# Performance work log

Hardware: AMD Instinct MI355X
Metric: run time of the kernel (lower is better)

The kernel has to match this reference:

```python
import jax, jax.numpy as jnp
import numpy as np

NUM_NODES = 100000
NUM_EDGES = 3_200_000
WALKS_PER_NODE = 4
WALK_LENGTH = 8
SKIP_FIRST = True


def setup_inputs() -> dict:
    key = jax.random.key(0)
    k1, k2, k3 = jax.random.split(key, 3)
    edge_index = jax.random.randint(k1, (2, NUM_EDGES), 0, NUM_NODES, dtype=jnp.int32)
    edge_weight = jax.random.uniform(k2, (NUM_EDGES,), dtype=jnp.float32)
    # one uniform per walker per step; S = NUM_NODES * WALKS_PER_NODE
    rand_unif = jax.random.uniform(k3, (NUM_NODES * WALKS_PER_NODE, WALK_LENGTH), dtype=jnp.float32)
    return {"edge_index": edge_index, "edge_weight": edge_weight, "rand_unif": rand_unif}


def _random_walk_edges(edge_index, rand_unif):
    """Returns added [2, S*L] edges (root -> walked node), int dtype."""
    row, col = edge_index[0], edge_index[1]
    # is_sorted=False path: sort edges by source to build CSR
    order = jnp.argsort(row)
    row_s = row[order]
    col_s = col[order]
    deg = jax.ops.segment_sum(jnp.ones_like(row_s), row_s, num_segments=NUM_NODES)  # [N]
    rowptr = jnp.concatenate([jnp.zeros((1,), deg.dtype), jnp.cumsum(deg)])  # [N+1]
    # start = all nodes, repeated walks_per_node times
    start = jnp.tile(jnp.arange(NUM_NODES, dtype=row.dtype), WALKS_PER_NODE)  # [S]

    def step(cur, u):
        d = deg[cur]  # [S]
        off = jnp.minimum((u * d.astype(u.dtype)).astype(cur.dtype), jnp.maximum(d - 1, 0))
        nxt = jnp.where(d > 0, col_s[rowptr[cur] + off], cur)  # stay if isolated
        return nxt, nxt

    _, walks = jax.lax.scan(step, start, rand_unif.T)  # [L_total, S]
    walks = walks.T  # [S, WALK_LENGTH] == n_id[:, 1:]
    k = 1 if SKIP_FIRST else 0  # skip_first drops the first-hop node (n_id[:, 2:])
    targets = walks[:, k:]  # [S, L]
    L = targets.shape[1]
    roots = jnp.broadcast_to(start[:, None], (start.shape[0], L))
    return jnp.stack([roots.reshape(-1), targets.reshape(-1)])  # [2, S*L]


def reference(edge_index, edge_weight, rand_unif):
    added = _random_walk_edges(edge_index, rand_unif)
    out_edge_index = jnp.concatenate([edge_index, added], axis=1)
    added_w = jnp.ones((added.shape[1],), edge_weight.dtype)
    out_edge_weight = jnp.concatenate([edge_weight, added_w])
    return out_edge_index, out_edge_weight
```

## Files before the change

kernel.cpp:

```cpp
#include <hip/hip_runtime.h>

#define ARW_N_NODES   100000
#define ARW_N_EDGES   3200000
#define ARW_N_WALKERS 400000
#define ARW_WLEN      8
#define ARW_LOUT      7
#define ARW_ROW_LEN   6000000
#define ARW_OUT_ELEMS 18000000

#define ARW_NB    256
#define ARW_RPB   392
#define ARW_NT    3125
#define ARW_TP    3136
#define ARW_TILE  1024
#define ARW_TPB   25

#define ARW_HT    0
#define ARW_BT    900000
#define ARW_TOT   1750000
#define ARW_CB    1760000
#define ARW_PD    1800000
#define ARW_P     6000000
#define ARW_COLS  12000000

__global__ void AddRandomWalkEdge_16896401342869_kernel() {}

__global__ __launch_bounds__(1024) void arw16896_thist(const int* __restrict__ row,
                                                       int* __restrict__ s) {
    __shared__ int h[ARW_TPB * 256];
    int tid = threadIdx.x;
    for (int x = tid; x < ARW_TPB * 256; x += 1024) h[x] = 0;
    __syncthreads();
    int base_e = blockIdx.x * (ARW_TPB * ARW_TILE) + tid;
    #pragma unroll
    for (int j = 0; j < ARW_TPB; j++)
        atomicAdd(&h[j * 256 + (row[base_e + j * 1024] / ARW_RPB)], 1);
    __syncthreads();
    for (int x = tid; x < ARW_TPB * ARW_NB; x += 1024) {
        int b = x / ARW_TPB, j = x % ARW_TPB;
        s[ARW_HT + b * ARW_TP + blockIdx.x * ARW_TPB + j] = h[j * 256 + b];
    }
}

__global__ __launch_bounds__(1024) void arw16896_btot(int* __restrict__ s) {
    __shared__ int wsum[16];
    int b = blockIdx.x, tid = threadIdx.x, lane = tid & 63, wid = tid >> 6;
    int acc = 0;
    for (int t = tid; t < ARW_NT; t += 1024) acc += s[ARW_HT + b * ARW_TP + t];
    #pragma unroll
    for (int off = 32; off > 0; off >>= 1) acc += __shfl_down(acc, off, 64);
    if (lane == 0) wsum[wid] = acc;
    __syncthreads();
    if (tid == 0) {
        int a = 0;
        #pragma unroll
        for (int w = 0; w < 16; w++) a += wsum[w];
        s[ARW_TOT + b] = a;
    }
}

__global__ __launch_bounds__(256) void arw16896_bbase(int* __restrict__ s) {
    __shared__ int sm[256];
    int tid = threadIdx.x;
    int v = s[ARW_TOT + tid];
    sm[tid] = v;
    __syncthreads();
    for (int off = 1; off < 256; off <<= 1) {
        int x = 0;
        if (tid >= off) x = sm[tid - off];
        __syncthreads();
        sm[tid] += x;
        __syncthreads();
    }
    s[ARW_CB + tid] = sm[tid] - v;
}

__global__ __launch_bounds__(1024) void arw16896_bscan2(int* __restrict__ s) {
    __shared__ int wsum[16];
    int b = blockIdx.x, tid = threadIdx.x, lane = tid & 63, wid = tid >> 6;
    int carry = s[ARW_CB + b];
    for (int c0 = 0; c0 < ARW_NT; c0 += 1024) {
        int t = c0 + tid;
        int v = (t < ARW_NT) ? s[ARW_HT + b * ARW_TP + t] : 0;
        int sv = v;
        #pragma unroll
        for (int off = 1; off < 64; off <<= 1) {
            int x = __shfl_up(sv, off, 64);
            if (lane >= off) sv += x;
        }
        if (lane == 63) wsum[wid] = sv;
        __syncthreads();
        int pre = 0, tot = 0;
        #pragma unroll
        for (int w = 0; w < 16; w++) {
            int x = wsum[w];
            if (w < wid) pre += x;
            tot += x;
        }
        if (t < ARW_NT) s[ARW_BT + b * ARW_TP + t] = carry + pre + sv - v;
        carry += tot;
        __syncthreads();
    }
}

__global__ __launch_bounds__(1024) void arw16896_part(const int* __restrict__ row,
                                                      const int* __restrict__ col,
                                                      int* __restrict__ s) {
    __shared__ unsigned W[16 * 256];
    int tid  = threadIdx.x;
    int wave = tid >> 6, lane = tid & 63;
    int e = blockIdx.x * ARW_TILE + tid;
    int r = row[e], cv = col[e];
    int b = r / ARW_RPB;
    int lr = r - b * ARW_RPB;
    W[tid] = 0; W[tid + 1024] = 0; W[tid + 2048] = 0; W[tid + 3072] = 0;
    __syncthreads();
    unsigned long long mask = ~0ULL;
    #pragma unroll
    for (int bit = 0; bit < 8; bit++) {
        unsigned long long bal = __ballot((b >> bit) & 1);
        mask &= ((b >> bit) & 1) ? bal : ~bal;
    }
    int rankw = __popcll(mask & ((1ULL << lane) - 1ULL));
    W[wave * 256 + b] = (unsigned)__popcll(mask);
    __syncthreads();
    int cross = 0;
    for (int w2 = 0; w2 < 16; w2++) {
        if (w2 >= wave) break;
        cross += (int)W[w2 * 256 + b];
    }
    int base = s[ARW_BT + b * ARW_TP + blockIdx.x];
    s[ARW_P + base + cross + rankw] = (lr << 17) | cv;
}

__global__ __launch_bounds__(1024) void arw16896_pass2(int* __restrict__ s) {
    __shared__ unsigned W[16 * 512];
    __shared__ int hist[512], pref[512], runc[512];
    int tid = threadIdx.x, lane = tid & 63, wave = tid >> 6;
    int b = blockIdx.x;
    int start = s[ARW_BT + b * ARW_TP];
    int end   = (b == ARW_NB - 1) ? ARW_N_EDGES : s[ARW_BT + (b + 1) * ARW_TP];
    int cnt = end - start;
    int rows0 = b * ARW_RPB;
    int nrows = ARW_N_NODES - rows0; if (nrows > ARW_RPB) nrows = ARW_RPB;

    if (tid < 512) hist[tid] = 0;
    __syncthreads();
    for (int k = tid; k < cnt; k += 1024)
        atomicAdd(&hist[(unsigned)s[ARW_P + start + k] >> 17], 1);
    __syncthreads();
    if (tid < 512) pref[tid] = hist[tid];
    __syncthreads();
    for (int off = 1; off < 512; off <<= 1) {
        int x = 0;
        if (tid < 512 && tid >= off) x = pref[tid - off];
        __syncthreads();
        if (tid < 512) pref[tid] += x;
        __syncthreads();
    }
    if (tid < 512) runc[tid] = 0;
    if (tid < nrows) {
        unsigned deg = (unsigned)hist[tid];
        unsigned rp  = (unsigned)(start + pref[tid] - hist[tid]);
        s[ARW_PD + rows0 + tid] = (int)((rp << 10) | deg);
    }
    __syncthreads();

    for (int c0 = 0; c0 < cnt; c0 += 1024) {
        int k = c0 + tid;
        int valid = (k < cnt) ? 1 : 0;
        unsigned p = valid ? (unsigned)s[ARW_P + start + k] : 0u;
        unsigned lr = p >> 17;
        #pragma unroll
        for (int j = 0; j < 8; j++) W[tid + j * 1024] = 0;
        __syncthreads();
        unsigned long long mask = ~0ULL;
        #pragma unroll
        for (int bit = 0; bit < 9; bit++) {
            unsigned long long bal = __ballot((lr >> bit) & 1u);
            mask &= ((lr >> bit) & 1u) ? bal : ~bal;
        }
        mask &= __ballot(valid);
        int rankw = __popcll(mask & ((1ULL << lane) - 1ULL));
        if (valid) W[wave * 512 + lr] = (unsigned)__popcll(mask);
        __syncthreads();
        if (valid) {
            int cross = 0;
            for (int w2 = 0; w2 < 16; w2++) {
                if (w2 >= wave) break;
                cross += (int)W[w2 * 512 + lr];
            }
            int pos = start + (pref[lr] - hist[lr]) + runc[lr] + cross + rankw;
            s[ARW_COLS + pos] = (int)(p & 0x1FFFFu);
        }
        __syncthreads();
        if (tid < 512) {
            int a = 0;
            #pragma unroll
            for (int w = 0; w < 16; w++) a += (int)W[w * 512 + tid];
            runc[tid] += a;
        }
        __syncthreads();
    }
}

__global__ __launch_bounds__(64) void arw16896_walk(const float* __restrict__ ru,
                                                    const int* __restrict__ s,
                                                    float* __restrict__ o) {
    __shared__ float tg[4 * 64 * ARW_LOUT];
    int tid = threadIdx.x;
    int v = blockIdx.x * 64 + tid;
    if (v < ARW_N_NODES) {
        float uu[4][8];
        int cur[4];
        #pragma unroll
        for (int k = 0; k < 4; k++) {
            const float4* rp4 = (const float4*)(ru + (size_t)(v + k * ARW_N_NODES) * 8);
            float4 ra = rp4[0], rb = rp4[1];
            uu[k][0] = ra.x; uu[k][1] = ra.y; uu[k][2] = ra.z; uu[k][3] = ra.w;
            uu[k][4] = rb.x; uu[k][5] = rb.y; uu[k][6] = rb.z; uu[k][7] = rb.w;
        }
        unsigned pd0 = (unsigned)s[ARW_PD + v];
        int d0  = (int)(pd0 & 1023u);
        int rp0 = (int)(pd0 >> 10);
        #pragma unroll
        for (int k = 0; k < 4; k++) {
            int off = (int)(uu[k][0] * (float)d0);
            if (off > d0 - 1) off = d0 - 1;
            int nxt = s[ARW_COLS + rp0 + off];
            cur[k] = (d0 > 0) ? nxt : v;
        }
        #pragma unroll
        for (int t = 1; t < ARW_WLEN; t++) {
            unsigned pdk[4];
            #pragma unroll
            for (int k = 0; k < 4; k++) pdk[k] = (unsigned)s[ARW_PD + cur[k]];
            #pragma unroll
            for (int k = 0; k < 4; k++) {
                int d = (int)(pdk[k] & 1023u);
                int off = (int)(uu[k][t] * (float)d);
                if (off > d - 1) off = d - 1;
                int nxt = s[ARW_COLS + (int)(pdk[k] >> 10) + off];
                cur[k] = (d > 0) ? nxt : cur[k];
                tg[k * (64 * ARW_LOUT) + tid * ARW_LOUT + (t - 1)] = (float)cur[k];
            }
        }
    }
    __syncthreads();
    int blkN = ARW_N_NODES - blockIdx.x * 64;
    if (blkN > 64) blkN = 64;
    int valid = blkN * ARW_LOUT;
    #pragma unroll
    for (int k = 0; k < 4; k++) {
        int base = ARW_ROW_LEN + ARW_N_EDGES +
                   (k * ARW_N_NODES + blockIdx.x * 64) * ARW_LOUT;
        for (int j = tid; j < valid; j += 64)
            o[base + j] = tg[k * (64 * ARW_LOUT) + j];
    }
}

__global__ __launch_bounds__(256) void arw16896_asm(const int* __restrict__ ei,
                                                    const float* __restrict__ wgt,
                                                    float* __restrict__ o) {
    int i4 = blockIdx.x * blockDim.x + threadIdx.x;
    if (i4 < ARW_N_EDGES / 4) {
        int4 r0 = ((const int4*)ei)[i4];
        int4 r1 = ((const int4*)(ei + ARW_N_EDGES))[i4];
        float4 wv = ((const float4*)wgt)[i4];
        ((float4*)o)[i4] = make_float4((float)r0.x, (float)r0.y, (float)r0.z, (float)r0.w);
        ((float4*)(o + ARW_ROW_LEN))[i4] =
            make_float4((float)r1.x, (float)r1.y, (float)r1.z, (float)r1.w);
        ((float4*)(o + 2 * ARW_ROW_LEN))[i4] = wv;
    }
    if (i4 < (ARW_N_WALKERS * ARW_LOUT) / 4) {
        int i = i4 * 4;
        float4 r;
        r.x = (float)(((i    ) / ARW_LOUT) % ARW_N_NODES);
        r.y = (float)(((i + 1) / ARW_LOUT) % ARW_N_NODES);
        r.z = (float)(((i + 2) / ARW_LOUT) % ARW_N_NODES);
        r.w = (float)(((i + 3) / ARW_LOUT) % ARW_N_NODES);
        ((float4*)(o + ARW_N_EDGES))[i4] = r;
        ((float4*)(o + 2 * ARW_ROW_LEN + ARW_N_EDGES))[i4] = make_float4(1.f, 1.f, 1.f, 1.f);
    }
}

extern "C" void kernel_launch(void* const* d_in, const int* in_sizes, int n_in,
                              void* d_out, int out_size, void* d_ws, size_t ws_size,
                              hipStream_t stream) {
    const int*   ei  = (const int*)d_in[0];
    const float* wgt = (const float*)d_in[1];
    const float* ru  = (const float*)d_in[2];
    int*   s = (int*)d_out;
    float* o = (float*)d_out;
    const int* row = ei;
    const int* col = ei + ARW_N_EDGES;

    arw16896_thist <<<ARW_NT / ARW_TPB, 1024, 0, stream>>>(row, s);
    arw16896_btot  <<<ARW_NB, 1024, 0, stream>>>(s);
    arw16896_bbase <<<1, 256, 0, stream>>>(s);
    arw16896_bscan2<<<ARW_NB, 1024, 0, stream>>>(s);
    arw16896_part  <<<ARW_NT, 1024, 0, stream>>>(row, col, s);
    arw16896_pass2 <<<ARW_NB, 1024, 0, stream>>>(s);
    arw16896_walk  <<<(ARW_N_NODES + 63) / 64, 64, 0, stream>>>(ru, s, o);
    arw16896_asm   <<<(ARW_N_EDGES / 4 + 255) / 256, 256, 0, stream>>>(ei, wgt, o);
}
```

Baseline: 252.8 us.

## Merge bucket scan passes, stage pass2 in LDS, fuse assembly into walk

The separate bucket-total kernel is folded into the per-bucket scan, which now produces local offsets plus a total. The partition kernel adds the global bucket base itself, which removes one kernel launch. The thist tiles-per-block count drops to 5 to get more blocks. pass2 stages its bucket's packed entries in shared memory so they are read from global memory once, and the W counters shrink to 16-bit. The walk kernel moves to 256-thread blocks and also writes the col-row conversion and the root indices, which trims the work of the assembly kernel. The larger shared memory footprint in pass2 and walk may lower occupancy.

```diff
diff --git a/kernel.cpp b/kernel.cpp
--- a/kernel.cpp
+++ b/kernel.cpp
@@ -13,7 +13,8 @@
 #define ARW_NT    3125
 #define ARW_TP    3136
 #define ARW_TILE  1024
-#define ARW_TPB   25
+#define ARW_TPB   5
+#define ARW_PMAX  14336
 
 #define ARW_HT    0
 #define ARW_BT    900000
@@ -42,21 +43,33 @@
     }
 }
 
-__global__ __launch_bounds__(1024) void arw16896_btot(int* __restrict__ s) {
+__global__ __launch_bounds__(1024) void arw16896_bscan2(int* __restrict__ s) {
     __shared__ int wsum[16];
     int b = blockIdx.x, tid = threadIdx.x, lane = tid & 63, wid = tid >> 6;
-    int acc = 0;
-    for (int t = tid; t < ARW_NT; t += 1024) acc += s[ARW_HT + b * ARW_TP + t];
-    #pragma unroll
-    for (int off = 32; off > 0; off >>= 1) acc += __shfl_down(acc, off, 64);
-    if (lane == 0) wsum[wid] = acc;
-    __syncthreads();
-    if (tid == 0) {
-        int a = 0;
-        #pragma unroll
-        for (int w = 0; w < 16; w++) a += wsum[w];
-        s[ARW_TOT + b] = a;
-    }
+    int carry = 0;
+    for (int c0 = 0; c0 < ARW_NT; c0 += 1024) {
+        int t = c0 + tid;
+        int v = (t < ARW_NT) ? s[ARW_HT + b * ARW_TP + t] : 0;
+        int sv = v;
+        #pragma unroll
+        for (int off = 1; off < 64; off <<= 1) {
+            int x = __shfl_up(sv, off, 64);
+            if (lane >= off) sv += x;
+        }
+        if (lane == 63) wsum[wid] = sv;
+        __syncthreads();
+        int pre = 0, tot = 0;
+        #pragma unroll
+        for (int w = 0; w < 16; w++) {
+            int x = wsum[w];
+            if (w < wid) pre += x;
+            tot += x;
+        }
+        if (t < ARW_NT) s[ARW_BT + b * ARW_TP + t] = carry + pre + sv - v;
+        carry += tot;
+        __syncthreads();
+    }
+    if (tid == 0) s[ARW_TOT + b] = carry;
 }
 
 __global__ __launch_bounds__(256) void arw16896_bbase(int* __restrict__ s) {
@@ -73,34 +86,6 @@
         __syncthreads();
     }
     s[ARW_CB + tid] = sm[tid] - v;
-}
-
-__global__ __launch_bounds__(1024) void arw16896_bscan2(int* __restrict__ s) {
-    __shared__ int wsum[16];
-    int b = blockIdx.x, tid = threadIdx.x, lane = tid & 63, wid = tid >> 6;
-    int carry = s[ARW_CB + b];
-    for (int c0 = 0; c0 < ARW_NT; c0 += 1024) {
-        int t = c0 + tid;
-        int v = (t < ARW_NT) ? s[ARW_HT + b * ARW_TP + t] : 0;
-        int sv = v;
-        #pragma unroll
-        for (int off = 1; off < 64; off <<= 1) {
-            int x = __shfl_up(sv, off, 64);
-            if (lane >= off) sv += x;
-        }
-        if (lane == 63) wsum[wid] = sv;
-        __syncthreads();
-        int pre = 0, tot = 0;
-        #pragma unroll
-        for (int w = 0; w < 16; w++) {
-            int x = wsum[w];
-            if (w < wid) pre += x;
-            tot += x;
-        }
-        if (t < ARW_NT) s[ARW_BT + b * ARW_TP + t] = carry + pre + sv - v;
-        carry += tot;
-        __syncthreads();
-    }
 }
 
 __global__ __launch_bounds__(1024) void arw16896_part(const int* __restrict__ row,
@@ -129,25 +114,31 @@
         if (w2 >= wave) break;
         cross += (int)W[w2 * 256 + b];
     }
-    int base = s[ARW_BT + b * ARW_TP + blockIdx.x];
+    int base = s[ARW_CB + b] + s[ARW_BT + b * ARW_TP + blockIdx.x];
     s[ARW_P + base + cross + rankw] = (lr << 17) | cv;
 }
 
 __global__ __launch_bounds__(1024) void arw16896_pass2(int* __restrict__ s) {
-    __shared__ unsigned W[16 * 512];
+    __shared__ int PL[ARW_PMAX];
+    __shared__ unsigned short W[16 * 512];
     __shared__ int hist[512], pref[512], runc[512];
     int tid = threadIdx.x, lane = tid & 63, wave = tid >> 6;
     int b = blockIdx.x;
-    int start = s[ARW_BT + b * ARW_TP];
-    int end   = (b == ARW_NB - 1) ? ARW_N_EDGES : s[ARW_BT + (b + 1) * ARW_TP];
+    int start = s[ARW_CB + b];
+    int end   = (b == ARW_NB - 1) ? ARW_N_EDGES : s[ARW_CB + b + 1];
     int cnt = end - start;
+    int staged = cnt < ARW_PMAX ? cnt : ARW_PMAX;
     int rows0 = b * ARW_RPB;
     int nrows = ARW_N_NODES - rows0; if (nrows > ARW_RPB) nrows = ARW_RPB;
 
+    for (int k = tid; k < staged; k += 1024) PL[k] = s[ARW_P + start + k];
     if (tid < 512) hist[tid] = 0;
     __syncthreads();
-    for (int k = tid; k < cnt; k += 1024)
-        atomicAdd(&hist[(unsigned)s[ARW_P + start + k] >> 17], 1);
+
+    for (int k = tid; k < cnt; k += 1024) {
+        unsigned p = (unsigned)(k < staged ? PL[k] : s[ARW_P + start + k]);
+        atomicAdd(&hist[p >> 17], 1);
+    }
     __syncthreads();
     if (tid < 512) pref[tid] = hist[tid];
     __syncthreads();
@@ -169,7 +160,8 @@
     for (int c0 = 0; c0 < cnt; c0 += 1024) {
         int k = c0 + tid;
         int valid = (k < cnt) ? 1 : 0;
-        unsigned p = valid ? (unsigned)s[ARW_P + start + k] : 0u;
+        unsigned p = 0u;
+        if (valid) p = (unsigned)(k < staged ? PL[k] : s[ARW_P + start + k]);
         unsigned lr = p >> 17;
         #pragma unroll
         for (int j = 0; j < 8; j++) W[tid + j * 1024] = 0;
@@ -182,7 +174,7 @@
         }
         mask &= __ballot(valid);
         int rankw = __popcll(mask & ((1ULL << lane) - 1ULL));
-        if (valid) W[wave * 512 + lr] = (unsigned)__popcll(mask);
+        if (valid) W[wave * 512 + lr] = (unsigned short)__popcll(mask);
         __syncthreads();
         if (valid) {
             int cross = 0;
@@ -204,12 +196,13 @@
     }
 }
 
-__global__ __launch_bounds__(64) void arw16896_walk(const float* __restrict__ ru,
-                                                    const int* __restrict__ s,
-                                                    float* __restrict__ o) {
-    __shared__ float tg[4 * 64 * ARW_LOUT];
+__global__ __launch_bounds__(256) void arw16896_walk(const float* __restrict__ ru,
+                                                     const int* __restrict__ ei,
+                                                     const int* __restrict__ s,
+                                                     float* __restrict__ o) {
+    __shared__ float tg[4 * 256 * ARW_LOUT];
     int tid = threadIdx.x;
-    int v = blockIdx.x * 64 + tid;
+    int v = blockIdx.x * 256 + tid;
     if (v < ARW_N_NODES) {
         float uu[4][8];
         int cur[4];
@@ -242,37 +235,29 @@
                 if (off > d - 1) off = d - 1;
                 int nxt = s[ARW_COLS + (int)(pdk[k] >> 10) + off];
                 cur[k] = (d > 0) ? nxt : cur[k];
-                tg[k * (64 * ARW_LOUT) + tid * ARW_LOUT + (t - 1)] = (float)cur[k];
+                tg[k * (256 * ARW_LOUT) + tid * ARW_LOUT + (t - 1)] = (float)cur[k];
             }
         }
     }
     __syncthreads();
-    int blkN = ARW_N_NODES - blockIdx.x * 64;
-    if (blkN > 64) blkN = 64;
+    int blkN = ARW_N_NODES - blockIdx.x * 256;
+    if (blkN > 256) blkN = 256;
     int valid = blkN * ARW_LOUT;
     #pragma unroll
     for (int k = 0; k < 4; k++) {
         int base = ARW_ROW_LEN + ARW_N_EDGES +
-                   (k * ARW_N_NODES + blockIdx.x * 64) * ARW_LOUT;
-        for (int j = tid; j < valid; j += 64)
-            o[base + j] = tg[k * (64 * ARW_LOUT) + j];
-    }
-}
-
-__global__ __launch_bounds__(256) void arw16896_asm(const int* __restrict__ ei,
-                                                    const float* __restrict__ wgt,
-                                                    float* __restrict__ o) {
-    int i4 = blockIdx.x * blockDim.x + threadIdx.x;
-    if (i4 < ARW_N_EDGES / 4) {
-        int4 r0 = ((const int4*)ei)[i4];
+                   (k * ARW_N_NODES + blockIdx.x * 256) * ARW_LOUT;
+        for (int j = tid; j < valid; j += 256)
+            o[base + j] = tg[k * (256 * ARW_LOUT) + j];
+    }
+    int gid = blockIdx.x * 256 + tid;
+    int stride = gridDim.x * 256;
+    for (int i4 = gid; i4 < ARW_N_EDGES / 4; i4 += stride) {
         int4 r1 = ((const int4*)(ei + ARW_N_EDGES))[i4];
-        float4 wv = ((const float4*)wgt)[i4];
-        ((float4*)o)[i4] = make_float4((float)r0.x, (float)r0.y, (float)r0.z, (float)r0.w);
         ((float4*)(o + ARW_ROW_LEN))[i4] =
             make_float4((float)r1.x, (float)r1.y, (float)r1.z, (float)r1.w);
-        ((float4*)(o + 2 * ARW_ROW_LEN))[i4] = wv;
-    }
-    if (i4 < (ARW_N_WALKERS * ARW_LOUT) / 4) {
+    }
+    for (int i4 = gid; i4 < (ARW_N_WALKERS * ARW_LOUT) / 4; i4 += stride) {
         int i = i4 * 4;
         float4 r;
         r.x = (float)(((i    ) / ARW_LOUT) % ARW_N_NODES);
@@ -280,6 +265,20 @@
         r.z = (float)(((i + 2) / ARW_LOUT) % ARW_N_NODES);
         r.w = (float)(((i + 3) / ARW_LOUT) % ARW_N_NODES);
         ((float4*)(o + ARW_N_EDGES))[i4] = r;
+    }
+}
+
+__global__ __launch_bounds__(256) void arw16896_asm(const int* __restrict__ ei,
+                                                    const float* __restrict__ wgt,
+                                                    float* __restrict__ o) {
+    int i4 = blockIdx.x * blockDim.x + threadIdx.x;
+    if (i4 < ARW_N_EDGES / 4) {
+        int4 r0 = ((const int4*)ei)[i4];
+        float4 wv = ((const float4*)wgt)[i4];
+        ((float4*)o)[i4] = make_float4((float)r0.x, (float)r0.y, (float)r0.z, (float)r0.w);
+        ((float4*)(o + 2 * ARW_ROW_LEN))[i4] = wv;
+    }
+    if (i4 < (ARW_N_WALKERS * ARW_LOUT) / 4) {
         ((float4*)(o + 2 * ARW_ROW_LEN + ARW_N_EDGES))[i4] = make_float4(1.f, 1.f, 1.f, 1.f);
     }
 }
@@ -296,11 +295,10 @@
     const int* col = ei + ARW_N_EDGES;
 
     arw16896_thist <<<ARW_NT / ARW_TPB, 1024, 0, stream>>>(row, s);
-    arw16896_btot  <<<ARW_NB, 1024, 0, stream>>>(s);
+    arw16896_bscan2<<<ARW_NB, 1024, 0, stream>>>(s);
     arw16896_bbase <<<1, 256, 0, stream>>>(s);
-    arw16896_bscan2<<<ARW_NB, 1024, 0, stream>>>(s);
     arw16896_part  <<<ARW_NT, 1024, 0, stream>>>(row, col, s);
     arw16896_pass2 <<<ARW_NB, 1024, 0, stream>>>(s);
-    arw16896_walk  <<<(ARW_N_NODES + 63) / 64, 64, 0, stream>>>(ru, s, o);
+    arw16896_walk  <<<(ARW_N_NODES + 255) / 256, 256, 0, stream>>>(ru, ei, s, o);
     arw16896_asm   <<<(ARW_N_EDGES / 4 + 255) / 256, 256, 0, stream>>>(ei, wgt, o);
 }
```

Result: faster. 234.8 us (-7.1%).
